# Optimization experiments

Hardware: AMD Instinct MI355X
Metric: run time of the kernel (lower is better)

The kernel has to match this reference:

```python
import jax, jax.numpy as jnp
import numpy as np

DIM = 1024
EPS = 1e-5


def setup_inputs() -> dict:
    key = jax.random.key(0)
    ks = jax.random.split(key, 7)
    C = DIM
    x = jax.random.normal(ks[0], (4, 4096, C), dtype=jnp.float32)
    norm_w = jnp.ones((C,), dtype=jnp.float32)
    norm_b = jnp.zeros((C,), dtype=jnp.float32)
    s = 1.0 / np.sqrt(C)
    qkv_w = jax.random.uniform(ks[1], (3 * C, C), dtype=jnp.float32, minval=-s, maxval=s)
    qkv_b = jax.random.uniform(ks[2], (3 * C,), dtype=jnp.float32, minval=-s, maxval=s)
    proj_w = jax.random.uniform(ks[3], (C, C), dtype=jnp.float32, minval=-s, maxval=s)
    proj_b = jax.random.uniform(ks[4], (C,), dtype=jnp.float32, minval=-s, maxval=s)
    return {"x": x, "norm_w": norm_w, "norm_b": norm_b, "qkv_w": qkv_w,
            "qkv_b": qkv_b, "proj_w": proj_w, "proj_b": proj_b}


def _layernorm(x, w, b):
    mu = jnp.mean(x, axis=-1, keepdims=True)
    var = jnp.mean(jnp.square(x - mu), axis=-1, keepdims=True)
    return (x - mu) * jax.lax.rsqrt(var + EPS) * w + b


def reference(x, norm_w, norm_b, qkv_w, qkv_b, proj_w, proj_b):
    B, T, C = x.shape
    residual = x
    h = _layernorm(x, norm_w, norm_b)
    qkv = jnp.einsum('btc,oc->bto', h, qkv_w) + qkv_b  # [B,T,3C]
    q, k, v = qkv[..., :C], qkv[..., C:2 * C], qkv[..., 2 * C:]
    attn = jnp.einsum('btc,bsc->bts', q, k) / jnp.sqrt(jnp.float32(C))  # raw QK^T, no softmax
    o = jnp.einsum('bts,bsc->btc', attn, v)
    o = jnp.einsum('btc,oc->bto', o, proj_w) + proj_b
    return residual + o  # dropout is identity in eval mode
```

## Files before the change

### kernel.cpp

```cpp
#include <hip/hip_runtime.h>

typedef _Float16 f16;
typedef _Float16 f16x4 __attribute__((ext_vector_type(4)));
typedef _Float16 f16x8 __attribute__((ext_vector_type(8)));
typedef float f32x4 __attribute__((ext_vector_type(4)));

#define AS1 __attribute__((address_space(1)))
#define AS3 __attribute__((address_space(3)))

__device__ __forceinline__ void gl_lds16(const f16* g, f16* l) {
  __builtin_amdgcn_global_load_lds((const AS1 void*)g, (AS3 void*)l, 16, 0, 0);
}

__global__ __launch_bounds__(256) void ln_kernel(const float* __restrict__ x,
                                                 const float* __restrict__ gw,
                                                 const float* __restrict__ gb,
                                                 f16* __restrict__ H,
                                                 float* __restrict__ hs) {
  if (blockIdx.x == 0) {
#pragma unroll
    for (int j = 0; j < 4; ++j)
      ((float4*)hs)[threadIdx.x + 256 * j] = make_float4(0.f, 0.f, 0.f, 0.f);
  }
  const int wv = threadIdx.x >> 6, lane = threadIdx.x & 63;
  const long row = (long)blockIdx.x * 4 + wv;
  const float* xr = x + row * 1024;
  float4 v[4];
  float s = 0.f, s2 = 0.f;
#pragma unroll
  for (int j = 0; j < 4; ++j) {
    v[j] = ((const float4*)xr)[lane + 64 * j];
    s  += v[j].x + v[j].y + v[j].z + v[j].w;
    s2 += v[j].x * v[j].x + v[j].y * v[j].y + v[j].z * v[j].z + v[j].w * v[j].w;
  }
#pragma unroll
  for (int off = 32; off > 0; off >>= 1) {
    s  += __shfl_xor(s, off);
    s2 += __shfl_xor(s2, off);
  }
  const float mu = s * (1.0f / 1024.0f);
  const float rstd = rsqrtf(s2 * (1.0f / 1024.0f) - mu * mu + 1e-5f);
#pragma unroll
  for (int j = 0; j < 4; ++j) {
    const float4 w4 = ((const float4*)gw)[lane + 64 * j];
    const float4 b4 = ((const float4*)gb)[lane + 64 * j];
    f16x4 h;
    h[0] = (f16)((v[j].x - mu) * rstd * w4.x + b4.x);
    h[1] = (f16)((v[j].y - mu) * rstd * w4.y + b4.y);
    h[2] = (f16)((v[j].z - mu) * rstd * w4.z + b4.z);
    h[3] = (f16)((v[j].w - mu) * rstd * w4.w + b4.w);
    *(f16x4*)(H + row * 1024 + (lane + 64 * j) * 4) = h;
  }
}

__global__ __launch_bounds__(256) void transpose_cs_kernel(const f16* __restrict__ H,
                                                           f16* __restrict__ Ht,
                                                           float* __restrict__ hs) {
  __shared__ f16 tile[64][68];
  __shared__ float csum[4][64];
  const int b = blockIdx.z;
  const long Hb  = (long)b * 4096 * 1024;
  const long Htb = (long)b * 1024 * 4096;
  const int t0 = blockIdx.y * 64, c0 = blockIdx.x * 64;
  const int tid = threadIdx.x;
  const int r = tid >> 2, g0 = tid & 3;
#pragma unroll
  for (int i = 0; i < 4; ++i) {
    const int g = g0 + i * 4;
    f16x4 v = *(const f16x4*)(H + Hb + (long)(t0 + r) * 1024 + c0 + g * 4);
    *(f16x4*)&tile[r][g * 4] = v;
  }
  __syncthreads();
  {
    const int cl = tid & 63, rg = tid >> 6;
    float s = 0.f;
#pragma unroll
    for (int rr = 0; rr < 16; ++rr) s += (float)tile[rg * 16 + rr][cl];
    csum[rg][cl] = s;
  }
#pragma unroll
  for (int i = 0; i < 4; ++i) {
    const int g = g0 + i * 4;
    f16x4 v;
    v[0] = tile[g * 4 + 0][r];
    v[1] = tile[g * 4 + 1][r];
    v[2] = tile[g * 4 + 2][r];
    v[3] = tile[g * 4 + 3][r];
    *(f16x4*)(Ht + Htb + (long)(c0 + r) * 4096 + t0 + g * 4) = v;
  }
  __syncthreads();
  if (tid < 64)
    atomicAdd(&hs[b * 1024 + c0 + tid],
              csum[0][tid] + csum[1][tid] + csum[2][tid] + csum[3][tid]);
}

__global__ __launch_bounds__(256) void transcast4(const float* __restrict__ qkv_w,
                                                  const float* __restrict__ proj_w,
                                                  f16* __restrict__ WT3,
                                                  f16* __restrict__ Wh,
                                                  f16* __restrict__ Ph) {
  const int z = blockIdx.z;
  __shared__ f16 tile[64][68];
  const int r0 = blockIdx.y * 64, c0 = blockIdx.x * 64;
  const int tid = threadIdx.x;
  const int r = tid >> 2, g0 = tid & 3;
  if (z == 3) {
#pragma unroll
    for (int i = 0; i < 4; ++i) {
      const int g = g0 + i * 4;
      float4 v = *(const float4*)(proj_w + (long)(r0 + r) * 1024 + c0 + g * 4);
      f16x4 h; h[0]=(f16)v.x; h[1]=(f16)v.y; h[2]=(f16)v.z; h[3]=(f16)v.w;
      *(f16x4*)(Ph + (long)(r0 + r) * 1024 + c0 + g * 4) = h;
    }
    return;
  }
  const float* W = qkv_w + (long)z * 1048576;
  f16* WT = WT3 + (long)z * 1048576;
#pragma unroll
  for (int i = 0; i < 4; ++i) {
    const int g = g0 + i * 4;
    float4 v = *(const float4*)(W + (long)(r0 + r) * 1024 + c0 + g * 4);
    f16x4 h; h[0]=(f16)v.x; h[1]=(f16)v.y; h[2]=(f16)v.z; h[3]=(f16)v.w;
    *(f16x4*)&tile[r][g * 4] = h;
    if (z >= 1)
      *(f16x4*)(Wh + (long)z * 1048576 + (long)(r0 + r) * 1024 + c0 + g * 4) = h;
  }
  __syncthreads();
#pragma unroll
  for (int i = 0; i < 4; ++i) {
    const int g = g0 + i * 4;
    f16x4 v;
    v[0] = tile[g * 4 + 0][r];
    v[1] = tile[g * 4 + 1][r];
    v[2] = tile[g * 4 + 2][r];
    v[3] = tile[g * 4 + 3][r];
    *(f16x4*)(WT + (long)(c0 + r) * 1024 + r0 + g * 4) = v;
  }
}

__device__ __forceinline__ float dot1024(const f16* __restrict__ row,
                                         const float* __restrict__ v) {
  const int lane = threadIdx.x & 63;
  float s = 0.f;
#pragma unroll
  for (int j = 0; j < 2; ++j) {
    const int d = (lane + 64 * j) * 8;
    f16x8 a = *(const f16x8*)(row + d);
    float4 h0 = *(const float4*)(v + d);
    float4 h1 = *(const float4*)(v + d + 4);
    s += (float)a[0] * h0.x + (float)a[1] * h0.y + (float)a[2] * h0.z + (float)a[3] * h0.w
       + (float)a[4] * h1.x + (float)a[5] * h1.y + (float)a[6] * h1.z + (float)a[7] * h1.w;
  }
#pragma unroll
  for (int off = 32; off > 0; off >>= 1) s += __shfl_down(s, off);
  return s;
}

__device__ __forceinline__ float dotf1024(const float* __restrict__ a,
                                          const float* __restrict__ v) {
  const int lane = threadIdx.x & 63;
  float s = 0.f;
#pragma unroll
  for (int j = 0; j < 4; ++j) {
    const int d = (lane + 64 * j) * 4;
    float4 x = *(const float4*)(a + d);
    float4 q = *(const float4*)(v + d);
    s += x.x * q.x + x.y * q.y + x.z * q.z + x.w * q.w;
  }
#pragma unroll
  for (int off = 32; off > 0; off >>= 1) s += __shfl_down(s, off);
  return s;
}

__global__ void gemv3a(const f16* __restrict__ WT3, const f16* __restrict__ Ph,
                       const float* __restrict__ qkv_b, float* __restrict__ ayd,
                       float* __restrict__ scal) {
  if (blockIdx.x == 3072) {
    float s = dotf1024(qkv_b + 1024, qkv_b);
    if ((threadIdx.x & 63) == 0) scal[4] = s;
    return;
  }
  const int which = blockIdx.x >> 10, m = blockIdx.x & 1023;
  const f16* row;
  const float* v;
  if (which == 0)      { row = WT3 + (long)m * 1024;            v = qkv_b + 1024; }
  else if (which == 1) { row = WT3 + 1048576 + (long)m * 1024;  v = qkv_b; }
  else                 { row = Ph + (long)m * 1024;             v = qkv_b + 2048; }
  float s = dot1024(row, v);
  if ((threadIdx.x & 63) == 0) ayd[which * 1024 + m] = s;
}

#define GP64_COMMON()                                        \
  const int tid = threadIdx.x;                               \
  const int wave = tid >> 6, lane = tid & 63;                \
  const int lr = lane & 15, lk = lane >> 4;                  \
  const int srow = tid >> 3;                                 \
  const int slc  = (tid & 7) ^ (srow & 7);                   \
  const int kc0 = ((lk) ^ (lr & 7)) * 8;                     \
  const int kc1 = ((4 + lk) ^ (lr & 7)) * 8;

#define FINE2_LOOP(NT_)                                                            \
  SBq(0, 0, 0); SBq(0, 0, 1); SBq(0, 0, 2); SBq(0, 0, 3);                          \
  SAq(0, 0, 0); SAq(0, 0, 2); SAq(0, 0, 1); SAq(0, 0, 3);                          \
  int cur = 0;                                                                     \
  for (int t = 0; t < (NT_); ++t) {                                                \
    const f16* asb = &As[cur][0];                                                  \
    const f16* bsb = &Bs[cur][0];                                                  \
    const int nb = cur ^ 1;                                                        \
    const bool st = (t + 1 < (NT_));                                               \
    f16x8 bf[4][2], af[2][2];                                                      \
    asm volatile("s_waitcnt vmcnt(2)" ::: "memory");                               \
    asm volatile("s_barrier" ::: "memory");                                        \
    _Pragma("unroll")                                                              \
    for (int ni = 0; ni < 4; ++ni) {                                               \
      bf[ni][0] = *(const f16x8*)(bsb + (wn * 64 + ni * 16 + lr) * 64 + kc0);      \
      bf[ni][1] = *(const f16x8*)(bsb + (wn * 64 + ni * 16 + lr) * 64 + kc1);      \
    }                                                                              \
    _Pragma("unroll")                                                              \
    for (int mi = 0; mi < 2; ++mi) {                                               \
      af[mi][0] = *(const f16x8*)(asb + (wm * 64 + mi * 16 + lr) * 64 + kc0);      \
      af[mi][1] = *(const f16x8*)(asb + (wm * 64 + mi * 16 + lr) * 64 + kc1);      \
    }                                                                              \
    if (st) { SBq(nb, t + 1, 0); SBq(nb, t + 1, 1); SBq(nb, t + 1, 2);             \
              SBq(nb, t + 1, 3); SAq(nb, t + 1, 0); SAq(nb, t + 1, 2); }           \
    asm volatile("s_waitcnt lgkmcnt(0)" ::: "memory");                             \
    __builtin_amdgcn_s_setprio(1);                                                 \
    _Pragma("unroll")                                                              \
    for (int ks = 0; ks < 2; ++ks)                                                 \
      _Pragma("unroll")                                                            \
      for (int mi = 0; mi < 2; ++mi)                                               \
        _Pragma("unroll")                                                          \
        for (int ni = 0; ni < 4; ++ni)                                             \
          acc[mi][ni] = __builtin_amdgcn_mfma_f32_16x16x32_f16(af[mi][ks],         \
                            bf[ni][ks], acc[mi][ni], 0, 0, 0);                     \
    __builtin_amdgcn_s_setprio(0);                                                 \
    asm volatile("s_barrier" ::: "memory");                                        \
    if (st) asm volatile("s_waitcnt vmcnt(6)" ::: "memory");                       \
    else    asm volatile("s_waitcnt vmcnt(0)" ::: "memory");                       \
    asm volatile("s_barrier" ::: "memory");                                        \
    _Pragma("unroll")                                                              \
    for (int mi = 0; mi < 2; ++mi) {                                               \
      af[mi][0] = *(const f16x8*)(asb + (wm * 64 + (mi + 2) * 16 + lr) * 64 + kc0);\
      af[mi][1] = *(const f16x8*)(asb + (wm * 64 + (mi + 2) * 16 + lr) * 64 + kc1);\
    }                                                                              \
    if (st) { SAq(nb, t + 1, 1); SAq(nb, t + 1, 3); }                              \
    asm volatile("s_waitcnt lgkmcnt(0)" ::: "memory");                             \
    __builtin_amdgcn_s_setprio(1);                                                 \
    _Pragma("unroll")                                                              \
    for (int ks = 0; ks < 2; ++ks)                                                 \
      _Pragma("unroll")                                                            \
      for (int mi = 0; mi < 2; ++mi)                                               \
        _Pragma("unroll")                                                          \
        for (int ni = 0; ni < 4; ++ni)                                             \
          acc[mi + 2][ni] = __builtin_amdgcn_mfma_f32_16x16x32_f16(af[mi][ks],     \
                                bf[ni][ks], acc[mi + 2][ni], 0, 0, 0);             \
    __builtin_amdgcn_s_setprio(0);                                                 \
    asm volatile("s_barrier" ::: "memory");                                        \
    cur ^= 1;                                                                      \
  }

__global__ __launch_bounds__(256) void gemmT1_g3b(
    const f16* __restrict__ U, const f16* __restrict__ Gh, f16* __restrict__ T1,
    const f16* __restrict__ PWv, const float* __restrict__ hs,
    const float* __restrict__ ayd, float* __restrict__ efz,
    float* __restrict__ scal) {
  GP64_COMMON();
  __shared__ __align__(16) f16 As[2][8192];
  __shared__ __align__(16) f16 Bs[2][8192];

  const int bid = blockIdx.x;
  if (bid >= 256) {
    const int u = (bid - 256) * 4 + wave;
    if (u >= 12288) {
      const int b = u - 12288;
      float s = dotf1024(hs + b * 1024, ayd + 1024);
      if (lane == 0) scal[b] = s;
      return;
    }
    const int sel = u >> 12, r = u & 4095;
    const int b = r >> 10, m = r & 1023;
    const f16* row;
    const float* v;
    if (sel == 0)      { row = U + (long)m * 1024;                       v = hs + b * 1024; }
    else if (sel == 1) { row = PWv + (long)m * 1024;                     v = hs + b * 1024; }
    else               { row = Gh + (long)b * 1048576 + (long)m * 1024;  v = ayd + 1024; }
    float s = dot1024(row, v);
    if (lane == 0) efz[sel * 4096 + r] = s;
    return;
  }

  const int ny = bid & 7, nx = (bid >> 3) & 7, b = bid >> 6;
  const int wm = wave >> 1, wn = wave & 1;
  const f16* Ab = U + (long)(ny * 128 + srow) * 1024 + slc * 8;
  const f16* Bb = Gh + (long)b * 1048576 + (long)(nx * 128 + srow) * 1024 + slc * 8;

  f32x4 zero = {0.f, 0.f, 0.f, 0.f};
  f32x4 acc[4][4];
#pragma unroll
  for (int mi = 0; mi < 4; ++mi)
#pragma unroll
    for (int ni = 0; ni < 4; ++ni) acc[mi][ni] = zero;

#define SAq(buf, kt, q) gl_lds16(Ab + (long)(q) * 32768 + (kt) * 64, &As[buf][(q) * 2048] + tid * 8)
#define SBq(buf, kt, q) gl_lds16(Bb + (long)(q) * 32768 + (kt) * 64, &Bs[buf][(q) * 2048] + tid * 8)
  FINE2_LOOP(16)
#undef SAq
#undef SBq

  f16* C = T1 + (long)b * 1048576;
  const int m0 = ny * 128 + wm * 64;
  const int n0 = nx * 128 + wn * 64;
#pragma unroll
  for (int mi = 0; mi < 4; ++mi)
#pragma unroll
    for (int ni = 0; ni < 4; ++ni)
#pragma unroll
      for (int j = 0; j < 4; ++j) {
        const int gm = m0 + mi * 16 + lk * 4 + j;
        const int gn = n0 + ni * 16 + lr;
        C[(long)gm * 1024 + gn] = (f16)acc[mi][ni][j];
      }
}

__global__ __launch_bounds__(256) void gemmW2_c2(
    const f16* __restrict__ PWv, const f16* __restrict__ T1, f16* __restrict__ T2,
    const float* __restrict__ ayd, const float* __restrict__ efz,
    const float* __restrict__ scal, const float* __restrict__ proj_b,
    float* __restrict__ c2v) {
  GP64_COMMON();
  __shared__ __align__(16) f16 As[2][8192];
  __shared__ __align__(16) f16 Bs[2][8192];

  const int bid = blockIdx.x;
  if (bid >= 256) {
    const int u = (bid - 256) * 4 + wave;
    const int b = u >> 10, c = u & 1023;
    float s = dot1024(PWv + (long)c * 1024, efz + 8192 + b * 1024);
    if (lane == 0) {
      const float d = ayd[2048 + c];
      c2v[b * 1024 + c] = (s + d * scal[b] + scal[4] * (efz[4096 + b * 1024 + c] + 4096.f * d))
                            * 0.03125f + proj_b[c];
    }
    return;
  }

  const int ny = bid & 7, nx = (bid >> 3) & 7, b = bid >> 6;
  const int wm = wave >> 1, wn = wave & 1;
  const f16* Ab = PWv + (long)(ny * 128 + srow) * 1024 + slc * 8;
  const f16* Bb = T1 + (long)b * 1048576 + (long)(nx * 128 + srow) * 1024 + slc * 8;

  f32x4 zero = {0.f, 0.f, 0.f, 0.f};
  f32x4 acc[4][4];
#pragma unroll
  for (int mi = 0; mi < 4; ++mi)
#pragma unroll
    for (int ni = 0; ni < 4; ++ni) acc[mi][ni] = zero;

#define SAq(buf, kt, q) gl_lds16(Ab + (long)(q) * 32768 + (kt) * 64, &As[buf][(q) * 2048] + tid * 8)
#define SBq(buf, kt, q) gl_lds16(Bb + (long)(q) * 32768 + (kt) * 64, &Bs[buf][(q) * 2048] + tid * 8)
  FINE2_LOOP(16)
#undef SAq
#undef SBq

  f16* C = T2 + (long)b * 1048576;
  const int m0 = ny * 128 + wm * 64;
  const int n0 = nx * 128 + wn * 64;
#pragma unroll
  for (int mi = 0; mi < 4; ++mi)
#pragma unroll
    for (int ni = 0; ni < 4; ++ni)
#pragma unroll
      for (int j = 0; j < 4; ++j) {
        const int gm = m0 + mi * 16 + lk * 4 + j;
        const int gn = n0 + ni * 16 + lr;
        const float dm = ayd[2048 + gm];
        const float fm = efz[4096 + b * 1024 + gm];
        const float en = efz[b * 1024 + gn];
        const float an = ayd[gn];
        float val = (acc[mi][ni][j] + dm * en + (fm + 4096.f * dm) * an) * 0.03125f;
        C[(long)gm * 1024 + gn] = (f16)val;
      }
}

__global__ __launch_bounds__(256) void gemmGUV(const f16* __restrict__ Ht,
                                               const f16* __restrict__ WT3,
                                               const f16* __restrict__ Ph,
                                               f16* __restrict__ part,
                                               f16* __restrict__ U,
                                               f16* __restrict__ PWv) {
  GP64_COMMON();
  const int wm = wave >> 1, wn = wave & 1;

  __shared__ __align__(16) f16 As[2][8192];
  __shared__ __align__(16) f16 Bs[2][8192];

  const int bid = blockIdx.x;
  const f16 *Ab, *Bb;
  long rs;
  int tileid = 0, zz = 0, selt = 0;
  if (bid < 576) {
    zz = bid & 15;
    tileid = bid >> 4;
    const int b = zz & 3, ks4 = zz >> 2;
    int ti = 0, trem = tileid;
    while (trem >= 8 - ti) { trem -= 8 - ti; ++ti; }
    const int tj = ti + trem;
    const f16* Hb = Ht + (long)b * 4194304;
    rs = 4096;
    Ab = Hb + (long)(ti * 128 + srow) * 4096 + (long)ks4 * 1024 + slc * 8;
    Bb = Hb + (long)(tj * 128 + srow) * 4096 + (long)ks4 * 1024 + slc * 8;
  } else {
    const int u = bid - 576;
    selt = (u >> 6) + 1;
    const int t = u & 63;
    const int ny = t >> 3, nxx = t & 7;
    const f16* A0 = (selt == 2) ? Ph : WT3;
    const f16* B0 = (selt == 2) ? (WT3 + 2097152) : (WT3 + 1048576);
    rs = 1024;
    Ab = A0 + (long)(ny * 128 + srow) * 1024 + slc * 8;
    Bb = B0 + (long)(nxx * 128 + srow) * 1024 + slc * 8;
  }

  f32x4 zero = {0.f, 0.f, 0.f, 0.f};
  f32x4 acc[4][4];
#pragma unroll
  for (int mi = 0; mi < 4; ++mi)
#pragma unroll
    for (int ni = 0; ni < 4; ++ni) acc[mi][ni] = zero;

#define SAq(buf, kt, q) gl_lds16(Ab + (long)(q) * 32 * rs + (kt) * 64, &As[buf][(q) * 2048] + tid * 8)
#define SBq(buf, kt, q) gl_lds16(Bb + (long)(q) * 32 * rs + (kt) * 64, &Bs[buf][(q) * 2048] + tid * 8)
  FINE2_LOOP(16)
#undef SAq
#undef SBq

  if (selt == 0) {
    f16* P = part + ((long)zz * 36 + tileid) * 16384;
#pragma unroll
    for (int mi = 0; mi < 4; ++mi)
#pragma unroll
      for (int ni = 0; ni < 4; ++ni)
#pragma unroll
        for (int j = 0; j < 4; ++j) {
          const int gm = wm * 64 + mi * 16 + lk * 4 + j;
          const int gn = wn * 64 + ni * 16 + lr;
          P[gm * 128 + gn] = (f16)acc[mi][ni][j];
        }
  } else {
    const int u = bid - 576;
    const int t = u & 63;
    const int ny = t >> 3, nxx = t & 7;
    f16* C = (selt == 2) ? PWv : U;
    const int m0 = ny * 128 + wm * 64;
    const int n0 = nxx * 128 + wn * 64;
#pragma unroll
    for (int mi = 0; mi < 4; ++mi)
#pragma unroll
      for (int ni = 0; ni < 4; ++ni)
#pragma unroll
        for (int j = 0; j < 4; ++j) {
          const int gm = m0 + mi * 16 + lk * 4 + j;
          const int gn = n0 + ni * 16 + lr;
          C[(long)gm * 1024 + gn] = (f16)acc[mi][ni][j];
        }
  }
}

__global__ __launch_bounds__(512) void gemm256f(
    const f16* __restrict__ A,
    const f16* __restrict__ Bw,
    const float* __restrict__ resid,
    const float* __restrict__ c2v,
    float* __restrict__ outF) {
  const int lin = blockIdx.y * 4 + blockIdx.x;
  const int xcd = lin & 7, slot = lin >> 3;
  const int ny = xcd * 8 + (slot >> 2);
  const int nx = slot & 3;
  const int bb = ny >> 4;

  GP64_COMMON();
  const int wm = wave >> 2, wn = wave & 3;

  __shared__ __align__(16) f16 As[2][16384];
  __shared__ __align__(16) f16 Bs[2][16384];

  const f16* Ab = A + (long)ny * 262144;
  const f16* Bb = Bw + (long)bb * 1048576 + (long)nx * 262144;
  const long offs = (long)srow * 1024 + slc * 8;

  f32x4 zero = {0.f, 0.f, 0.f, 0.f};
  f32x4 acc[8][4];
#pragma unroll
  for (int mi = 0; mi < 8; ++mi)
#pragma unroll
    for (int ni = 0; ni < 4; ++ni) acc[mi][ni] = zero;

#define SA(buf, kt, q) gl_lds16(Ab + offs + (long)(q) * 65536 + (kt) * 64, &As[buf][(q) * 4096] + tid * 8)
#define SB(buf, kt, q) gl_lds16(Bb + offs + (long)(q) * 65536 + (kt) * 64, &Bs[buf][(q) * 4096] + tid * 8)

#define RD_BF(dst, bsb, kc)                                                       \
  _Pragma("unroll")                                                               \
  for (int ni = 0; ni < 4; ++ni)                                                  \
    dst[ni] = *(const f16x8*)((bsb) + (wn * 64 + ni * 16 + lr) * 64 + (kc));
#define RD_AF(dst, asb, mh, kc)                                                   \
  _Pragma("unroll")                                                               \
  for (int mi = 0; mi < 4; ++mi)                                                  \
    dst[mi] = *(const f16x8*)((asb) + (wm * 128 + (mh) * 64 + mi * 16 + lr) * 64 + (kc));
#define MF16(af_, bf_, mo)                                                        \
  __builtin_amdgcn_s_setprio(1);                                                  \
  _Pragma("unroll")                                                               \
  for (int mi = 0; mi < 4; ++mi)                                                  \
    _Pragma("unroll")                                                             \
    for (int ni = 0; ni < 4; ++ni)                                                \
      acc[(mo) + mi][ni] = __builtin_amdgcn_mfma_f32_16x16x32_f16(af_[mi], bf_[ni], \
                                                                  acc[(mo) + mi][ni], 0, 0, 0); \
  __builtin_amdgcn_s_setprio(0);

  const int nt = 16;
  SB(0, 0, 0); SB(0, 0, 1); SB(0, 0, 2); SB(0, 0, 3);
  SA(0, 0, 0); SA(0, 0, 2); SA(0, 0, 1); SA(0, 0, 3);

  int cur = 0;
  for (int t = 0; t < nt; ++t) {
    const f16* asb = &As[cur][0];
    const f16* bsb = &Bs[cur][0];
    const int nb = cur ^ 1;
    const bool st = (t + 1 < nt);
    f16x8 bf[4], af[4];

    asm volatile("s_waitcnt vmcnt(2)" ::: "memory");
    asm volatile("s_barrier" ::: "memory");
    RD_BF(bf, bsb, kc0);
    RD_AF(af, asb, 0, kc0);
    if (st) { SB(nb, t + 1, 0); SB(nb, t + 1, 1); }
    asm volatile("s_waitcnt lgkmcnt(0)" ::: "memory");
    MF16(af, bf, 0);
    asm volatile("s_barrier" ::: "memory");

    if (st) asm volatile("s_waitcnt vmcnt(2)" ::: "memory");
    else    asm volatile("s_waitcnt vmcnt(0)" ::: "memory");
    asm volatile("s_barrier" ::: "memory");
    RD_AF(af, asb, 1, kc0);
    if (st) { SB(nb, t + 1, 2); SB(nb, t + 1, 3); }
    asm volatile("s_waitcnt lgkmcnt(0)" ::: "memory");
    MF16(af, bf, 4);
    asm volatile("s_barrier" ::: "memory");

    RD_BF(bf, bsb, kc1);
    RD_AF(af, asb, 0, kc1);
    if (st) { SA(nb, t + 1, 0); SA(nb, t + 1, 2); }
    asm volatile("s_waitcnt lgkmcnt(0)" ::: "memory");
    MF16(af, bf, 0);
    asm volatile("s_barrier" ::: "memory");

    RD_AF(af, asb, 1, kc1);
    if (st) { SA(nb, t + 1, 1); SA(nb, t + 1, 3); }
    asm volatile("s_waitcnt lgkmcnt(0)" ::: "memory");
    MF16(af, bf, 4);
    asm volatile("s_barrier" ::: "memory");

    cur ^= 1;
  }
#undef SA
#undef SB
#undef RD_BF
#undef RD_AF
#undef MF16

  asm volatile("s_waitcnt vmcnt(0)" ::: "memory");
  asm volatile("s_barrier" ::: "memory");

  float* weps = ((float*)&As[0][0]) + wave * 1088;
  const int m0 = ny * 256 + wm * 128;
  const int n0 = nx * 256 + wn * 64;
  const int err = lane >> 3;
  const int ecc = (lane & 7) * 4;
  float4 cc2[2];
#pragma unroll
  for (int q = 0; q < 2; ++q)
    cc2[q] = *(const float4*)&c2v[bb * 1024 + n0 + ecc + 32 * q];

#pragma unroll
  for (int mi = 0; mi < 8; ++mi) {
#pragma unroll
    for (int ni = 0; ni < 4; ++ni)
#pragma unroll
      for (int j = 0; j < 4; ++j)
        weps[(lk * 4 + j) * 68 + ni * 16 + lr] = acc[mi][ni][j];
    asm volatile("s_waitcnt lgkmcnt(0)" ::: "memory");
#pragma unroll
    for (int h = 0; h < 2; ++h)
#pragma unroll
      for (int q = 0; q < 2; ++q) {
        const int rr = err + 8 * h;
        const int cc = ecc + 32 * q;
        float4 o = *(const float4*)&weps[rr * 68 + cc];
        const long gbase = (long)(m0 + mi * 16 + rr) * 1024 + n0 + cc;
        const float4 rv = *(const float4*)&resid[gbase];
        float4 ov;
        ov.x = o.x + rv.x + cc2[q].x;
        ov.y = o.y + rv.y + cc2[q].y;
        ov.z = o.z + rv.z + cc2[q].z;
        ov.w = o.w + rv.w + cc2[q].w;
        *(float4*)&outF[gbase] = ov;
      }
  }
}

__global__ __launch_bounds__(256) void treduce(const f16* __restrict__ part,
                                               f16* __restrict__ Gh) {
  const int tileid = blockIdx.x, b = blockIdx.y;
  int ti = 0, trem = tileid;
  while (trem >= 8 - ti) { trem -= 8 - ti; ++ti; }
  const int tj = ti + trem;
  __shared__ f16 tl[128][132];
  const int tid = threadIdx.x;
  f16* Gb = Gh + (long)b * 1048576;
#pragma unroll
  for (int it = 0; it < 16; ++it) {
    const int e = it * 1024 + tid * 4;
    const int r = e >> 7, c = e & 127;
    f16x4 p0 = *(const f16x4*)(part + ((long)(0 * 4 + b) * 36 + tileid) * 16384 + e);
    f16x4 p1 = *(const f16x4*)(part + ((long)(1 * 4 + b) * 36 + tileid) * 16384 + e);
    f16x4 p2 = *(const f16x4*)(part + ((long)(2 * 4 + b) * 36 + tileid) * 16384 + e);
    f16x4 p3 = *(const f16x4*)(part + ((long)(3 * 4 + b) * 36 + tileid) * 16384 + e);
    f16x4 sv;
#pragma unroll
    for (int j = 0; j < 4; ++j)
      sv[j] = (f16)((float)p0[j] + (float)p1[j] + (float)p2[j] + (float)p3[j]);
    *(f16x4*)(Gb + (long)(ti * 128 + r) * 1024 + tj * 128 + c) = sv;
    *(f16x4*)&tl[r][c] = sv;
  }
  if (ti != tj) {
    __syncthreads();
#pragma unroll
    for (int it = 0; it < 16; ++it) {
      const int e = it * 1024 + tid * 4;
      const int r = e >> 7, c = e & 127;
      f16x4 v;
      v[0] = tl[c + 0][r];
      v[1] = tl[c + 1][r];
      v[2] = tl[c + 2][r];
      v[3] = tl[c + 3][r];
      *(f16x4*)(Gb + (long)(tj * 128 + r) * 1024 + ti * 128 + c) = v;
    }
  }
}

extern "C" void kernel_launch(void* const* d_in, const int* in_sizes, int n_in,
                              void* d_out, int out_size, void* d_ws, size_t ws_size,
                              hipStream_t stream) {
  const float* x      = (const float*)d_in[0];
  const float* norm_w = (const float*)d_in[1];
  const float* norm_b = (const float*)d_in[2];
  const float* qkv_w  = (const float*)d_in[3];
  const float* qkv_b  = (const float*)d_in[4];
  const float* proj_w = (const float*)d_in[5];
  const float* proj_b = (const float*)d_in[6];
  float* out = (float*)d_out;
  char* ws = (char*)d_ws;

  const size_t OFF_H    = 0;
  const size_t OFF_HT   = 33554432;
  const size_t OFF_T1   = 33554432;
  const size_t OFF_T2   = 41943040;
  const size_t OFF_WH   = 67108864;
  const size_t OFF_PH   = 73400320;
  const size_t OFF_WT3  = 75497472;
  const size_t OFF_U    = 81788928;
  const size_t OFF_PWV  = 83886080;
  const size_t OFF_GH   = 85983232;
  const size_t OFF_PART = 94371840;
  const size_t OFF_HS   = 115343360;
  const size_t OFF_AYD  = 115392512;
  const size_t OFF_SCAL = 115404800;
  const size_t OFF_EFZ  = 115405824;
  const size_t OFF_C2   = 115471360;

  f16* H    = (f16*)(ws + OFF_H);
  f16* Ht   = (f16*)(ws + OFF_HT);
  f16* T1   = (f16*)(ws + OFF_T1);
  f16* T2   = (f16*)(ws + OFF_T2);
  f16* Wh   = (f16*)(ws + OFF_WH);
  f16* Ph   = (f16*)(ws + OFF_PH);
  f16* WT3  = (f16*)(ws + OFF_WT3);
  f16* U    = (f16*)(ws + OFF_U);
  f16* PWv  = (f16*)(ws + OFF_PWV);
  f16* Gh   = (f16*)(ws + OFF_GH);
  f16* part = (f16*)(ws + OFF_PART);
  float* hs   = (float*)(ws + OFF_HS);
  float* ayd  = (float*)(ws + OFF_AYD);
  float* scal = (float*)(ws + OFF_SCAL);
  float* efz  = (float*)(ws + OFF_EFZ);
  float* c2v  = (float*)(ws + OFF_C2);

  transcast4<<<dim3(16, 16, 4), 256, 0, stream>>>(qkv_w, proj_w, WT3, Wh, Ph);
  gemv3a<<<dim3(3073), 64, 0, stream>>>(WT3, Ph, qkv_b, ayd, scal);

  ln_kernel<<<dim3(4096), 256, 0, stream>>>(x, norm_w, norm_b, H, hs);
  transpose_cs_kernel<<<dim3(16, 64, 4), 256, 0, stream>>>(H, Ht, hs);

  gemmGUV<<<dim3(704), 256, 0, stream>>>(Ht, WT3, Ph, part, U, PWv);
  treduce<<<dim3(36, 4), 256, 0, stream>>>(part, Gh);

  gemmT1_g3b<<<dim3(3329), 256, 0, stream>>>(U, Gh, T1, PWv, hs, ayd, efz, scal);
  gemmW2_c2<<<dim3(1280), 256, 0, stream>>>(PWv, T1, T2, ayd, efz, scal, proj_b, c2v);

  gemm256f<<<dim3(4, 64), 512, 0, stream>>>(H, T2, x, c2v, out);
}
```

Baseline: 178.5 us.

## Merge weight prep into layernorm and gemv into transpose launches

Folds the weight transpose/cast work into the layernorm kernel as extra blocks, and the bias GEMV work into the transpose/column-sum kernel as extra blocks. This cuts four launches down to two and lets the independent weight-prep and activation-prep work share the GPU at once instead of running one after another. It also drops the unused Wh fp16 copy of qkv_w, which removes some write traffic. The cost is a heavier kernel with more shared-memory and register use per block, and the gemv blocks now pack four waves per block.

```diff
diff --git a/kernel.cpp b/kernel.cpp
--- a/kernel.cpp
+++ b/kernel.cpp
@@ -12,18 +12,92 @@
   __builtin_amdgcn_global_load_lds((const AS1 void*)g, (AS3 void*)l, 16, 0, 0);
 }
 
-__global__ __launch_bounds__(256) void ln_kernel(const float* __restrict__ x,
-                                                 const float* __restrict__ gw,
-                                                 const float* __restrict__ gb,
-                                                 f16* __restrict__ H,
-                                                 float* __restrict__ hs) {
-  if (blockIdx.x == 0) {
+__device__ __forceinline__ float dot1024(const f16* __restrict__ row,
+                                         const float* __restrict__ v) {
+  const int lane = threadIdx.x & 63;
+  float s = 0.f;
+#pragma unroll
+  for (int j = 0; j < 2; ++j) {
+    const int d = (lane + 64 * j) * 8;
+    f16x8 a = *(const f16x8*)(row + d);
+    float4 h0 = *(const float4*)(v + d);
+    float4 h1 = *(const float4*)(v + d + 4);
+    s += (float)a[0] * h0.x + (float)a[1] * h0.y + (float)a[2] * h0.z + (float)a[3] * h0.w
+       + (float)a[4] * h1.x + (float)a[5] * h1.y + (float)a[6] * h1.z + (float)a[7] * h1.w;
+  }
+#pragma unroll
+  for (int off = 32; off > 0; off >>= 1) s += __shfl_down(s, off);
+  return s;
+}
+
+__device__ __forceinline__ float dotf1024(const float* __restrict__ a,
+                                          const float* __restrict__ v) {
+  const int lane = threadIdx.x & 63;
+  float s = 0.f;
+#pragma unroll
+  for (int j = 0; j < 4; ++j) {
+    const int d = (lane + 64 * j) * 4;
+    float4 x = *(const float4*)(a + d);
+    float4 q = *(const float4*)(v + d);
+    s += x.x * q.x + x.y * q.y + x.z * q.z + x.w * q.w;
+  }
+#pragma unroll
+  for (int off = 32; off > 0; off >>= 1) s += __shfl_down(s, off);
+  return s;
+}
+
+__global__ __launch_bounds__(256) void prep_kernel(
+    const float* __restrict__ x, const float* __restrict__ gw,
+    const float* __restrict__ gb, f16* __restrict__ H, float* __restrict__ hs,
+    const float* __restrict__ qkv_w, const float* __restrict__ proj_w,
+    f16* __restrict__ WT3, f16* __restrict__ Ph) {
+  const int bid = blockIdx.x;
+  const int tid = threadIdx.x;
+  if (bid >= 4096) {
+    const int u = bid - 4096;
+    const int z = u >> 8;
+    const int r0 = ((u >> 4) & 15) * 64, c0 = (u & 15) * 64;
+    const int r = tid >> 2, g0 = tid & 3;
+    if (z == 3) {
+#pragma unroll
+      for (int i = 0; i < 4; ++i) {
+        const int g = g0 + i * 4;
+        float4 v = *(const float4*)(proj_w + (long)(r0 + r) * 1024 + c0 + g * 4);
+        f16x4 h; h[0]=(f16)v.x; h[1]=(f16)v.y; h[2]=(f16)v.z; h[3]=(f16)v.w;
+        *(f16x4*)(Ph + (long)(r0 + r) * 1024 + c0 + g * 4) = h;
+      }
+      return;
+    }
+    __shared__ f16 tile[64][68];
+    const float* W = qkv_w + (long)z * 1048576;
+    f16* WT = WT3 + (long)z * 1048576;
+#pragma unroll
+    for (int i = 0; i < 4; ++i) {
+      const int g = g0 + i * 4;
+      float4 v = *(const float4*)(W + (long)(r0 + r) * 1024 + c0 + g * 4);
+      f16x4 h; h[0]=(f16)v.x; h[1]=(f16)v.y; h[2]=(f16)v.z; h[3]=(f16)v.w;
+      *(f16x4*)&tile[r][g * 4] = h;
+    }
+    __syncthreads();
+#pragma unroll
+    for (int i = 0; i < 4; ++i) {
+      const int g = g0 + i * 4;
+      f16x4 v;
+      v[0] = tile[g * 4 + 0][r];
+      v[1] = tile[g * 4 + 1][r];
+      v[2] = tile[g * 4 + 2][r];
+      v[3] = tile[g * 4 + 3][r];
+      *(f16x4*)(WT + (long)(c0 + r) * 1024 + r0 + g * 4) = v;
+    }
+    return;
+  }
+  if (bid == 0) {
 #pragma unroll
     for (int j = 0; j < 4; ++j)
-      ((float4*)hs)[threadIdx.x + 256 * j] = make_float4(0.f, 0.f, 0.f, 0.f);
-  }
-  const int wv = threadIdx.x >> 6, lane = threadIdx.x & 63;
-  const long row = (long)blockIdx.x * 4 + wv;
+      ((float4*)hs)[tid + 256 * j] = make_float4(0.f, 0.f, 0.f, 0.f);
+  }
+  const int wv = tid >> 6, lane = tid & 63;
+  const long row = (long)bid * 4 + wv;
   const float* xr = x + row * 1024;
   float4 v[4];
   float s = 0.f, s2 = 0.f;
@@ -53,16 +127,38 @@
   }
 }
 
-__global__ __launch_bounds__(256) void transpose_cs_kernel(const f16* __restrict__ H,
-                                                           f16* __restrict__ Ht,
-                                                           float* __restrict__ hs) {
+__global__ __launch_bounds__(256) void tcgemv_kernel(
+    const f16* __restrict__ H, f16* __restrict__ Ht, float* __restrict__ hs,
+    const f16* __restrict__ WT3, const f16* __restrict__ Ph,
+    const float* __restrict__ qkv_b, float* __restrict__ ayd,
+    float* __restrict__ scal) {
+  const int bid = blockIdx.x;
+  const int tid = threadIdx.x;
+  if (bid >= 4096) {
+    const int wave = tid >> 6, lane = tid & 63;
+    const int u = (bid - 4096) * 4 + wave;
+    if (u > 3072) return;
+    if (u == 3072) {
+      float s = dotf1024(qkv_b + 1024, qkv_b);
+      if (lane == 0) scal[4] = s;
+      return;
+    }
+    const int which = u >> 10, m = u & 1023;
+    const f16* row;
+    const float* v;
+    if (which == 0)      { row = WT3 + (long)m * 1024;            v = qkv_b + 1024; }
+    else if (which == 1) { row = WT3 + 1048576 + (long)m * 1024;  v = qkv_b; }
+    else                 { row = Ph + (long)m * 1024;             v = qkv_b + 2048; }
+    float s = dot1024(row, v);
+    if (lane == 0) ayd[which * 1024 + m] = s;
+    return;
+  }
   __shared__ f16 tile[64][68];
   __shared__ float csum[4][64];
-  const int b = blockIdx.z;
+  const int b = bid >> 10;
   const long Hb  = (long)b * 4096 * 1024;
   const long Htb = (long)b * 1024 * 4096;
-  const int t0 = blockIdx.y * 64, c0 = blockIdx.x * 64;
-  const int tid = threadIdx.x;
+  const int t0 = ((bid >> 4) & 63) * 64, c0 = (bid & 15) * 64;
   const int r = tid >> 2, g0 = tid & 3;
 #pragma unroll
   for (int i = 0; i < 4; ++i) {
@@ -92,102 +188,6 @@
   if (tid < 64)
     atomicAdd(&hs[b * 1024 + c0 + tid],
               csum[0][tid] + csum[1][tid] + csum[2][tid] + csum[3][tid]);
-}
-
-__global__ __launch_bounds__(256) void transcast4(const float* __restrict__ qkv_w,
-                                                  const float* __restrict__ proj_w,
-                                                  f16* __restrict__ WT3,
-                                                  f16* __restrict__ Wh,
-                                                  f16* __restrict__ Ph) {
-  const int z = blockIdx.z;
-  __shared__ f16 tile[64][68];
-  const int r0 = blockIdx.y * 64, c0 = blockIdx.x * 64;
-  const int tid = threadIdx.x;
-  const int r = tid >> 2, g0 = tid & 3;
-  if (z == 3) {
-#pragma unroll
-    for (int i = 0; i < 4; ++i) {
-      const int g = g0 + i * 4;
-      float4 v = *(const float4*)(proj_w + (long)(r0 + r) * 1024 + c0 + g * 4);
-      f16x4 h; h[0]=(f16)v.x; h[1]=(f16)v.y; h[2]=(f16)v.z; h[3]=(f16)v.w;
-      *(f16x4*)(Ph + (long)(r0 + r) * 1024 + c0 + g * 4) = h;
-    }
-    return;
-  }
-  const float* W = qkv_w + (long)z * 1048576;
-  f16* WT = WT3 + (long)z * 1048576;
-#pragma unroll
-  for (int i = 0; i < 4; ++i) {
-    const int g = g0 + i * 4;
-    float4 v = *(const float4*)(W + (long)(r0 + r) * 1024 + c0 + g * 4);
-    f16x4 h; h[0]=(f16)v.x; h[1]=(f16)v.y; h[2]=(f16)v.z; h[3]=(f16)v.w;
-    *(f16x4*)&tile[r][g * 4] = h;
-    if (z >= 1)
-      *(f16x4*)(Wh + (long)z * 1048576 + (long)(r0 + r) * 1024 + c0 + g * 4) = h;
-  }
-  __syncthreads();
-#pragma unroll
-  for (int i = 0; i < 4; ++i) {
-    const int g = g0 + i * 4;
-    f16x4 v;
-    v[0] = tile[g * 4 + 0][r];
-    v[1] = tile[g * 4 + 1][r];
-    v[2] = tile[g * 4 + 2][r];
-    v[3] = tile[g * 4 + 3][r];
-    *(f16x4*)(WT + (long)(c0 + r) * 1024 + r0 + g * 4) = v;
-  }
-}
-
-__device__ __forceinline__ float dot1024(const f16* __restrict__ row,
-                                         const float* __restrict__ v) {
-  const int lane = threadIdx.x & 63;
-  float s = 0.f;
-#pragma unroll
-  for (int j = 0; j < 2; ++j) {
-    const int d = (lane + 64 * j) * 8;
-    f16x8 a = *(const f16x8*)(row + d);
-    float4 h0 = *(const float4*)(v + d);
-    float4 h1 = *(const float4*)(v + d + 4);
-    s += (float)a[0] * h0.x + (float)a[1] * h0.y + (float)a[2] * h0.z + (float)a[3] * h0.w
-       + (float)a[4] * h1.x + (float)a[5] * h1.y + (float)a[6] * h1.z + (float)a[7] * h1.w;
-  }
-#pragma unroll
-  for (int off = 32; off > 0; off >>= 1) s += __shfl_down(s, off);
-  return s;
-}
-
-__device__ __forceinline__ float dotf1024(const float* __restrict__ a,
-                                          const float* __restrict__ v) {
-  const int lane = threadIdx.x & 63;
-  float s = 0.f;
-#pragma unroll
-  for (int j = 0; j < 4; ++j) {
-    const int d = (lane + 64 * j) * 4;
-    float4 x = *(const float4*)(a + d);
-    float4 q = *(const float4*)(v + d);
-    s += x.x * q.x + x.y * q.y + x.z * q.z + x.w * q.w;
-  }
-#pragma unroll
-  for (int off = 32; off > 0; off >>= 1) s += __shfl_down(s, off);
-  return s;
-}
-
-__global__ void gemv3a(const f16* __restrict__ WT3, const f16* __restrict__ Ph,
-                       const float* __restrict__ qkv_b, float* __restrict__ ayd,
-                       float* __restrict__ scal) {
-  if (blockIdx.x == 3072) {
-    float s = dotf1024(qkv_b + 1024, qkv_b);
-    if ((threadIdx.x & 63) == 0) scal[4] = s;
-    return;
-  }
-  const int which = blockIdx.x >> 10, m = blockIdx.x & 1023;
-  const f16* row;
-  const float* v;
-  if (which == 0)      { row = WT3 + (long)m * 1024;            v = qkv_b + 1024; }
-  else if (which == 1) { row = WT3 + 1048576 + (long)m * 1024;  v = qkv_b; }
-  else                 { row = Ph + (long)m * 1024;             v = qkv_b + 2048; }
-  float s = dot1024(row, v);
-  if ((threadIdx.x & 63) == 0) ayd[which * 1024 + m] = s;
 }
 
 #define GP64_COMMON()                                        \
@@ -664,7 +664,6 @@
   const size_t OFF_HT   = 33554432;
   const size_t OFF_T1   = 33554432;
   const size_t OFF_T2   = 41943040;
-  const size_t OFF_WH   = 67108864;
   const size_t OFF_PH   = 73400320;
   const size_t OFF_WT3  = 75497472;
   const size_t OFF_U    = 81788928;
@@ -681,7 +680,6 @@
   f16* Ht   = (f16*)(ws + OFF_HT);
   f16* T1   = (f16*)(ws + OFF_T1);
   f16* T2   = (f16*)(ws + OFF_T2);
-  f16* Wh   = (f16*)(ws + OFF_WH);
   f16* Ph   = (f16*)(ws + OFF_PH);
   f16* WT3  = (f16*)(ws + OFF_WT3);
   f16* U    = (f16*)(ws + OFF_U);
@@ -694,11 +692,9 @@
   float* efz  = (float*)(ws + OFF_EFZ);
   float* c2v  = (float*)(ws + OFF_C2);
 
-  transcast4<<<dim3(16, 16, 4), 256, 0, stream>>>(qkv_w, proj_w, WT3, Wh, Ph);
-  gemv3a<<<dim3(3073), 64, 0, stream>>>(WT3, Ph, qkv_b, ayd, scal);
-
-  ln_kernel<<<dim3(4096), 256, 0, stream>>>(x, norm_w, norm_b, H, hs);
-  transpose_cs_kernel<<<dim3(16, 64, 4), 256, 0, stream>>>(H, Ht, hs);
+  prep_kernel<<<dim3(5120), 256, 0, stream>>>(x, norm_w, norm_b, H, hs,
+                                              qkv_w, proj_w, WT3, Ph);
+  tcgemv_kernel<<<dim3(4865), 256, 0, stream>>>(H, Ht, hs, WT3, Ph, qkv_b, ayd, scal);
 
   gemmGUV<<<dim3(704), 256, 0, stream>>>(Ht, WT3, Ph, part, U, PWv);
   treduce<<<dim3(36, 4), 256, 0, stream>>>(part, Gh);
```

New measurement: 177.4 us. About the same (-0.6%).
